# Kernel tuning notes

Hardware: AMD Instinct MI355X
Metric: run time of the kernel (lower is better)

## Reference

```python
import jax, jax.numpy as jnp
import numpy as np

SIGMA = 0.5
KS = 5  # gaussian kernel size, covers > 4*sigma


def _gauss_kernel():
    x = jnp.arange(KS, dtype=jnp.float32) - (KS // 2)
    g = jnp.exp(-(x ** 2) / (2.0 * SIGMA ** 2))
    k2 = jnp.outer(g, g)
    return k2 / k2.sum()


def setup_inputs() -> dict:
    key = jax.random.key(0)
    k1, k2, k3, k4 = jax.random.split(key, 4)
    B, K, H, W = 64, 17, 128, 128
    heatmap = jax.random.normal(k1, (B, K, H, W), dtype=jnp.float32)
    tx = jax.random.randint(k2, (B, K), 0, W)
    ty = jax.random.randint(k3, (B, K), 0, H)
    vis = jax.random.randint(k4, (B, K), 0, 2)
    targets = jnp.stack([tx, ty, vis], axis=-1).astype(jnp.float32)  # [B,K,3] = (x, y, visible)
    return {"heatmap": heatmap, "targets": targets}


def reference(heatmap, targets):
    B, K, H, W = heatmap.shape
    # log-softmax over flattened spatial dims
    logp = jax.nn.log_softmax(heatmap.reshape(B, K, H * W), axis=2).reshape(B, K, H, W)

    t = jnp.round(targets).astype(jnp.int32)
    visible = (t[..., 2] > 0).astype(logp.dtype)  # [B,K]
    tx, ty = t[..., 0], t[..., 1]

    # one-hot 2D heatmap at (ty, tx): [B,K,H,W]
    oh = ((jnp.arange(H)[:, None] == ty[..., None, None]) &
          (jnp.arange(W)[None, :] == tx[..., None, None])).astype(jnp.float32)

    # depthwise gaussian smoothing ('same' zero padding)
    kern = _gauss_kernel().reshape(1, 1, KS, KS)
    tgt = jax.lax.conv_general_dilated(
        oh.reshape(B * K, 1, H, W), kern,
        window_strides=(1, 1), padding='SAME',
        dimension_numbers=('NCHW', 'OIHW', 'NCHW')).reshape(B, K, H, W)

    # KLDiv pointwise: y*(log y - x); zero where y == 0 (torch convention)
    safe_t = jnp.where(tgt > 0, tgt, 1.0)
    elem = jnp.where(tgt > 0, tgt * (jnp.log(safe_t) - logp), 0.0)
    per_bk = elem.sum(axis=(-2, -1))  # [B,K]

    n_vis = jnp.maximum(visible.sum(), 1.0)
    loss = jnp.sum(per_bk * visible) / n_vis  # batchmean over visible keypoints
    return loss
```

## Files before the change

kernel.cpp:

```cpp
#include <hip/hip_runtime.h>
#include <math.h>

constexpr int Hc     = 128;
constexpr int Wc     = 128;
constexpr int HWc    = Hc * Wc;
constexpr int NBK    = 64 * 17;
constexpr int NCHUNK = 4;
constexpr int CHUNK  = HWc / NCHUNK;
constexpr int NBLK   = NBK * NCHUNK;

constexpr float E2_1 = 0.13533528323661270f;
constexpr float E2_4 = 3.3546262790251185e-4f;
constexpr float S1F  = 1.0f + 2.0f * E2_1 + 2.0f * E2_4;
constexpr float INVN = 1.0f / (S1F * S1F);

__device__ __forceinline__ float gfac(int d) {
    const int a = d < 0 ? -d : d;
    return a == 0 ? 1.0f : (a == 1 ? E2_1 : E2_4);
}

__global__ __launch_bounds__(256) void kl_chunk(const float* __restrict__ hm,
                                                const float* __restrict__ tg,
                                                float* __restrict__ part) {
    const int bx    = blockIdx.x;
    const int bk    = bx >> 2;
    const int chunk = bx & 3;
    const int tid   = threadIdx.x;

    const float4* __restrict__ base4 =
        reinterpret_cast<const float4*>(hm + (size_t)bk * HWc + (size_t)chunk * CHUNK);

    float s0 = 0.f, s1 = 0.f, s2 = 0.f, s3 = 0.f;
#pragma unroll
    for (int c = 0; c < 4; ++c) {
        const float4 v = base4[c * 256 + tid];
        s0 += __expf(v.x); s1 += __expf(v.y);
        s2 += __expf(v.z); s3 += __expf(v.w);
    }
    float s = (s0 + s1) + (s2 + s3);

    float gh = 0.f;
    if (tid < 25) {
        const int dy = tid / 5 - 2;
        const int dx = tid % 5 - 2;
        const int tx = __float2int_rn(tg[bk * 3 + 0]) + dx;
        const int ty = __float2int_rn(tg[bk * 3 + 1]) + dy;
        const int r0 = chunk * (Hc / NCHUNK);
        if (tx >= 0 && tx < Wc && ty >= r0 && ty < r0 + Hc / NCHUNK)
            gh = gfac(dx) * gfac(dy) * INVN * hm[(size_t)bk * HWc + ty * Wc + tx];
    }

#pragma unroll
    for (int off = 32; off; off >>= 1) s += __shfl_xor(s, off);
#pragma unroll
    for (int off = 16; off; off >>= 1) gh += __shfl_xor(gh, off);

    __shared__ float ss[4];
    const int wave = tid >> 6;
    if ((tid & 63) == 0) ss[wave] = s;
    __syncthreads();
    if (tid == 0) {
        part[bx]        = ss[0] + ss[1] + ss[2] + ss[3];
        part[NBLK + bx] = gh;
    }
}

__global__ __launch_bounds__(1024) void kl_final(const float* __restrict__ part,
                                                 const float* __restrict__ tg,
                                                 float* __restrict__ out) {
    const int tid = threadIdx.x;
    const float LOGN = 2.0f * __logf(S1F);

    float acc = 0.f, nv = 0.f;
    for (int i = tid; i < NBK; i += 1024) {
        const float4 sv = *reinterpret_cast<const float4*>(part + 4 * i);
        const float4 gv = *reinterpret_cast<const float4*>(part + NBLK + 4 * i);
        const float S   = (sv.x + sv.y) + (sv.z + sv.w);
        const float gh  = (gv.x + gv.y) + (gv.z + gv.w);
        const float lse = __logf(S);

        const int tx  = __float2int_rn(tg[3 * i + 0]);
        const int ty  = __float2int_rn(tg[3 * i + 1]);
        const int vis = __float2int_rn(tg[3 * i + 2]) > 0;

        float cg = 0.f, cglg = 0.f;
#pragma unroll
        for (int w = 0; w < 25; ++w) {
            const int dy = w / 5 - 2;
            const int dx = w % 5 - 2;
            const int x = tx + dx, y = ty + dy;
            if (x >= 0 && x < Wc && y >= 0 && y < Hc) {
                const float g = gfac(dx) * gfac(dy) * INVN;
                cg   += g;
                cglg += g * (-2.f * (float)(dx * dx + dy * dy) - LOGN);
            }
        }
        const float per = cglg - gh + lse * cg;
        acc += vis ? per : 0.f;
        nv  += vis ? 1.f : 0.f;
    }

#pragma unroll
    for (int off = 32; off; off >>= 1) {
        acc += __shfl_xor(acc, off);
        nv  += __shfl_xor(nv,  off);
    }
    __shared__ float sa[16], sn[16];
    const int wave = tid >> 6;
    if ((tid & 63) == 0) { sa[wave] = acc; sn[wave] = nv; }
    __syncthreads();
    if (tid == 0) {
        float a = 0.f, n = 0.f;
#pragma unroll
        for (int w = 0; w < 16; ++w) { a += sa[w]; n += sn[w]; }
        out[0] = a / fmaxf(n, 1.f);
    }
}

extern "C" void kernel_launch(void* const* d_in, const int* in_sizes, int n_in,
                              void* d_out, int out_size, void* d_ws, size_t ws_size,
                              hipStream_t stream) {
    const float* heatmap = (const float*)d_in[0];
    const float* targets = (const float*)d_in[1];
    float* part = (float*)d_ws;
    float* out  = (float*)d_out;

    kl_chunk<<<NBLK, 256, 0, stream>>>(heatmap, targets, part);
    kl_final<<<1, 1024, 0, stream>>>(part, targets, out);
}
```

Measured before the change: 19.46 us.

## Fuse chunk and final kernels into one cooperative launch with grid sync

Merges the two kernels into a single cooperative kernel. Each 1024-thread block now handles four whole (b,k) maps, computes the per-keypoint loss in-block, and writes one partial per block. After a grid-wide sync, block 0 reduces the partials and the visible count. This removes the second kernel launch and the small serial tail, at the cost of grid-sync overhead and a smaller grid (272 blocks) with more work per thread.

```diff
diff --git a/kernel.cpp b/kernel.cpp
--- a/kernel.cpp
+++ b/kernel.cpp
@@ -1,13 +1,15 @@
 #include <hip/hip_runtime.h>
+#include <hip/hip_cooperative_groups.h>
 #include <math.h>
 
-constexpr int Hc     = 128;
-constexpr int Wc     = 128;
-constexpr int HWc    = Hc * Wc;
-constexpr int NBK    = 64 * 17;
-constexpr int NCHUNK = 4;
-constexpr int CHUNK  = HWc / NCHUNK;
-constexpr int NBLK   = NBK * NCHUNK;
+namespace cg = cooperative_groups;
+
+constexpr int Hc   = 128;
+constexpr int Wc   = 128;
+constexpr int HWc  = Hc * Wc;
+constexpr int NBK  = 64 * 17;
+constexpr int RPB  = 4;
+constexpr int NBLK = NBK / RPB;
 
 constexpr float E2_1 = 0.13533528323661270f;
 constexpr float E2_4 = 3.3546262790251185e-4f;
@@ -19,34 +21,36 @@
     return a == 0 ? 1.0f : (a == 1 ? E2_1 : E2_4);
 }
 
-__global__ __launch_bounds__(256) void kl_chunk(const float* __restrict__ hm,
-                                                const float* __restrict__ tg,
-                                                float* __restrict__ part) {
-    const int bx    = blockIdx.x;
-    const int bk    = bx >> 2;
-    const int chunk = bx & 3;
-    const int tid   = threadIdx.x;
+__global__ __launch_bounds__(1024, 8) void kl_all(const float* __restrict__ hm,
+                                                  const float* __restrict__ tg,
+                                                  float* __restrict__ part,
+                                                  float* __restrict__ out) {
+    const int blk     = blockIdx.x;
+    const int tid     = threadIdx.x;
+    const int row     = tid >> 8;
+    const int lane256 = tid & 255;
+    const int bk      = blk * RPB + row;
+    const int wave    = tid >> 6;
 
     const float4* __restrict__ base4 =
-        reinterpret_cast<const float4*>(hm + (size_t)bk * HWc + (size_t)chunk * CHUNK);
+        reinterpret_cast<const float4*>(hm + (size_t)bk * HWc);
 
     float s0 = 0.f, s1 = 0.f, s2 = 0.f, s3 = 0.f;
-#pragma unroll
-    for (int c = 0; c < 4; ++c) {
-        const float4 v = base4[c * 256 + tid];
+#pragma unroll 4
+    for (int c = 0; c < 16; ++c) {
+        const float4 v = base4[c * 256 + lane256];
         s0 += __expf(v.x); s1 += __expf(v.y);
         s2 += __expf(v.z); s3 += __expf(v.w);
     }
     float s = (s0 + s1) + (s2 + s3);
 
     float gh = 0.f;
-    if (tid < 25) {
-        const int dy = tid / 5 - 2;
-        const int dx = tid % 5 - 2;
+    if (lane256 < 25) {
+        const int dy = lane256 / 5 - 2;
+        const int dx = lane256 % 5 - 2;
         const int tx = __float2int_rn(tg[bk * 3 + 0]) + dx;
         const int ty = __float2int_rn(tg[bk * 3 + 1]) + dy;
-        const int r0 = chunk * (Hc / NCHUNK);
-        if (tx >= 0 && tx < Wc && ty >= r0 && ty < r0 + Hc / NCHUNK)
+        if (tx >= 0 && tx < Wc && ty >= 0 && ty < Hc)
             gh = gfac(dx) * gfac(dy) * INVN * hm[(size_t)bk * HWc + ty * Wc + tx];
     }
 
@@ -55,35 +59,21 @@
 #pragma unroll
     for (int off = 16; off; off >>= 1) gh += __shfl_xor(gh, off);
 
-    __shared__ float ss[4];
-    const int wave = tid >> 6;
+    __shared__ float ss[16];
+    __shared__ float rowres[RPB];
     if ((tid & 63) == 0) ss[wave] = s;
     __syncthreads();
-    if (tid == 0) {
-        part[bx]        = ss[0] + ss[1] + ss[2] + ss[3];
-        part[NBLK + bx] = gh;
-    }
-}
 
-__global__ __launch_bounds__(1024) void kl_final(const float* __restrict__ part,
-                                                 const float* __restrict__ tg,
-                                                 float* __restrict__ out) {
-    const int tid = threadIdx.x;
-    const float LOGN = 2.0f * __logf(S1F);
-
-    float acc = 0.f, nv = 0.f;
-    for (int i = tid; i < NBK; i += 1024) {
-        const float4 sv = *reinterpret_cast<const float4*>(part + 4 * i);
-        const float4 gv = *reinterpret_cast<const float4*>(part + NBLK + 4 * i);
-        const float S   = (sv.x + sv.y) + (sv.z + sv.w);
-        const float gh  = (gv.x + gv.y) + (gv.z + gv.w);
+    if (lane256 == 0) {
+        const float S   = ss[4 * row] + ss[4 * row + 1] + ss[4 * row + 2] + ss[4 * row + 3];
         const float lse = __logf(S);
 
-        const int tx  = __float2int_rn(tg[3 * i + 0]);
-        const int ty  = __float2int_rn(tg[3 * i + 1]);
-        const int vis = __float2int_rn(tg[3 * i + 2]) > 0;
+        const int tx  = __float2int_rn(tg[bk * 3 + 0]);
+        const int ty  = __float2int_rn(tg[bk * 3 + 1]);
+        const int vis = __float2int_rn(tg[bk * 3 + 2]) > 0;
 
-        float cg = 0.f, cglg = 0.f;
+        const float LOGN = 2.0f * __logf(S1F);
+        float cgs = 0.f, cglg = 0.f;
 #pragma unroll
         for (int w = 0; w < 25; ++w) {
             const int dy = w / 5 - 2;
@@ -91,29 +81,37 @@
             const int x = tx + dx, y = ty + dy;
             if (x >= 0 && x < Wc && y >= 0 && y < Hc) {
                 const float g = gfac(dx) * gfac(dy) * INVN;
-                cg   += g;
+                cgs  += g;
                 cglg += g * (-2.f * (float)(dx * dx + dy * dy) - LOGN);
             }
         }
-        const float per = cglg - gh + lse * cg;
-        acc += vis ? per : 0.f;
-        nv  += vis ? 1.f : 0.f;
+        rowres[row] = vis ? (cglg - gh + lse * cgs) : 0.f;
     }
+    __syncthreads();
+    if (tid == 0)
+        part[blk] = (rowres[0] + rowres[1]) + (rowres[2] + rowres[3]);
+
+    cg::this_grid().sync();
+    if (blk != 0) return;
+
+    float a  = (tid < NBLK) ? part[tid] : 0.f;
+    float nv = (tid < NBK && __float2int_rn(tg[3 * tid + 2]) > 0) ? 1.f : 0.f;
+    if (tid < NBK - 1024)
+        nv += (__float2int_rn(tg[3 * (tid + 1024) + 2]) > 0) ? 1.f : 0.f;
 
 #pragma unroll
     for (int off = 32; off; off >>= 1) {
-        acc += __shfl_xor(acc, off);
-        nv  += __shfl_xor(nv,  off);
+        a  += __shfl_xor(a,  off);
+        nv += __shfl_xor(nv, off);
     }
     __shared__ float sa[16], sn[16];
-    const int wave = tid >> 6;
-    if ((tid & 63) == 0) { sa[wave] = acc; sn[wave] = nv; }
+    if ((tid & 63) == 0) { sa[wave] = a; sn[wave] = nv; }
     __syncthreads();
     if (tid == 0) {
-        float a = 0.f, n = 0.f;
+        a = 0.f; nv = 0.f;
 #pragma unroll
-        for (int w = 0; w < 16; ++w) { a += sa[w]; n += sn[w]; }
-        out[0] = a / fmaxf(n, 1.f);
+        for (int w = 0; w < 16; ++w) { a += sa[w]; nv += sn[w]; }
+        out[0] = a / fmaxf(nv, 1.f);
     }
 }
 
@@ -125,6 +123,7 @@
     float* part = (float*)d_ws;
     float* out  = (float*)d_out;
 
-    kl_chunk<<<NBLK, 256, 0, stream>>>(heatmap, targets, part);
-    kl_final<<<1, 1024, 0, stream>>>(part, targets, out);
+    void* args[] = {(void*)&heatmap, (void*)&targets, (void*)&part, (void*)&out};
+    hipLaunchCooperativeKernel((const void*)kl_all, dim3(NBLK), dim3(1024),
+                               args, 0, stream);
 }
```

Result: slower. 57.02 us (+193.0%).

## Fuse chunk and final kernels into one kernel with atomic accumulation

Applied to the files above, without the earlier changes.

Each block now handles a whole (b,k) heatmap instead of a quarter. It computes the log-sum-exp, the target gather and the per-keypoint loss in the block, then atomically adds the result scaled by 1/n_visible into the output. The second reduction kernel is gone, replaced by a memset plus per-block atomics, and every block recounts visible keypoints with one wave. The grid has 4x fewer blocks, each with 4x more work, which may reduce latency hiding, and float atomics make the summation order nondeterministic.

```diff
diff --git a/kernel.cpp b/kernel.cpp
--- a/kernel.cpp
+++ b/kernel.cpp
@@ -1,13 +1,10 @@
 #include <hip/hip_runtime.h>
 #include <math.h>
 
-constexpr int Hc     = 128;
-constexpr int Wc     = 128;
-constexpr int HWc    = Hc * Wc;
-constexpr int NBK    = 64 * 17;
-constexpr int NCHUNK = 4;
-constexpr int CHUNK  = HWc / NCHUNK;
-constexpr int NBLK   = NBK * NCHUNK;
+constexpr int Hc  = 128;
+constexpr int Wc  = 128;
+constexpr int HWc = Hc * Wc;
+constexpr int NBK = 64 * 17;
 
 constexpr float E2_1 = 0.13533528323661270f;
 constexpr float E2_4 = 3.3546262790251185e-4f;
@@ -19,20 +16,20 @@
     return a == 0 ? 1.0f : (a == 1 ? E2_1 : E2_4);
 }
 
-__global__ __launch_bounds__(256) void kl_chunk(const float* __restrict__ hm,
-                                                const float* __restrict__ tg,
-                                                float* __restrict__ part) {
-    const int bx    = blockIdx.x;
-    const int bk    = bx >> 2;
-    const int chunk = bx & 3;
-    const int tid   = threadIdx.x;
+__global__ __launch_bounds__(256) void kl_one(const float* __restrict__ hm,
+                                              const float* __restrict__ tg,
+                                              float* __restrict__ out) {
+    const int bk   = blockIdx.x;
+    const int tid  = threadIdx.x;
+    const int lane = tid & 63;
+    const int wave = tid >> 6;
 
     const float4* __restrict__ base4 =
-        reinterpret_cast<const float4*>(hm + (size_t)bk * HWc + (size_t)chunk * CHUNK);
+        reinterpret_cast<const float4*>(hm + (size_t)bk * HWc);
 
     float s0 = 0.f, s1 = 0.f, s2 = 0.f, s3 = 0.f;
 #pragma unroll
-    for (int c = 0; c < 4; ++c) {
+    for (int c = 0; c < 16; ++c) {
         const float4 v = base4[c * 256 + tid];
         s0 += __expf(v.x); s1 += __expf(v.y);
         s2 += __expf(v.z); s3 += __expf(v.w);
@@ -45,75 +42,57 @@
         const int dx = tid % 5 - 2;
         const int tx = __float2int_rn(tg[bk * 3 + 0]) + dx;
         const int ty = __float2int_rn(tg[bk * 3 + 1]) + dy;
-        const int r0 = chunk * (Hc / NCHUNK);
-        if (tx >= 0 && tx < Wc && ty >= r0 && ty < r0 + Hc / NCHUNK)
+        if (tx >= 0 && tx < Wc && ty >= 0 && ty < Hc)
             gh = gfac(dx) * gfac(dy) * INVN * hm[(size_t)bk * HWc + ty * Wc + tx];
     }
 
+    float nv = 0.f;
+    if (wave == 1) {
 #pragma unroll
-    for (int off = 32; off; off >>= 1) s += __shfl_xor(s, off);
-#pragma unroll
-    for (int off = 16; off; off >>= 1) gh += __shfl_xor(gh, off);
-
-    __shared__ float ss[4];
-    const int wave = tid >> 6;
-    if ((tid & 63) == 0) ss[wave] = s;
-    __syncthreads();
-    if (tid == 0) {
-        part[bx]        = ss[0] + ss[1] + ss[2] + ss[3];
-        part[NBLK + bx] = gh;
-    }
-}
-
-__global__ __launch_bounds__(1024) void kl_final(const float* __restrict__ part,
-                                                 const float* __restrict__ tg,
-                                                 float* __restrict__ out) {
-    const int tid = threadIdx.x;
-    const float LOGN = 2.0f * __logf(S1F);
-
-    float acc = 0.f, nv = 0.f;
-    for (int i = tid; i < NBK; i += 1024) {
-        const float4 sv = *reinterpret_cast<const float4*>(part + 4 * i);
-        const float4 gv = *reinterpret_cast<const float4*>(part + NBLK + 4 * i);
-        const float S   = (sv.x + sv.y) + (sv.z + sv.w);
-        const float gh  = (gv.x + gv.y) + (gv.z + gv.w);
-        const float lse = __logf(S);
-
-        const int tx  = __float2int_rn(tg[3 * i + 0]);
-        const int ty  = __float2int_rn(tg[3 * i + 1]);
-        const int vis = __float2int_rn(tg[3 * i + 2]) > 0;
-
-        float cg = 0.f, cglg = 0.f;
-#pragma unroll
-        for (int w = 0; w < 25; ++w) {
-            const int dy = w / 5 - 2;
-            const int dx = w % 5 - 2;
-            const int x = tx + dx, y = ty + dy;
-            if (x >= 0 && x < Wc && y >= 0 && y < Hc) {
-                const float g = gfac(dx) * gfac(dy) * INVN;
-                cg   += g;
-                cglg += g * (-2.f * (float)(dx * dx + dy * dy) - LOGN);
-            }
-        }
-        const float per = cglg - gh + lse * cg;
-        acc += vis ? per : 0.f;
-        nv  += vis ? 1.f : 0.f;
+        for (int i = 0; i < NBK / 64; ++i)
+            nv += (__float2int_rn(tg[3 * (lane + 64 * i) + 2]) > 0) ? 1.f : 0.f;
     }
 
 #pragma unroll
     for (int off = 32; off; off >>= 1) {
-        acc += __shfl_xor(acc, off);
-        nv  += __shfl_xor(nv,  off);
+        s  += __shfl_xor(s,  off);
+        gh += __shfl_xor(gh, off);
+        nv += __shfl_xor(nv, off);
     }
-    __shared__ float sa[16], sn[16];
-    const int wave = tid >> 6;
-    if ((tid & 63) == 0) { sa[wave] = acc; sn[wave] = nv; }
+
+    __shared__ float ss[4];
+    __shared__ float sG, sNV;
+    if (lane == 0) {
+        ss[wave] = s;
+        if (wave == 0) sG  = gh;
+        if (wave == 1) sNV = nv;
+    }
     __syncthreads();
+
     if (tid == 0) {
-        float a = 0.f, n = 0.f;
+        const int vis = __float2int_rn(tg[bk * 3 + 2]) > 0;
+        if (vis) {
+            const float S   = (ss[0] + ss[1]) + (ss[2] + ss[3]);
+            const float lse = __logf(S);
+            const int tx = __float2int_rn(tg[bk * 3 + 0]);
+            const int ty = __float2int_rn(tg[bk * 3 + 1]);
+
+            const float LOGN = 2.0f * __logf(S1F);
+            float cg = 0.f, cglg = 0.f;
 #pragma unroll
-        for (int w = 0; w < 16; ++w) { a += sa[w]; n += sn[w]; }
-        out[0] = a / fmaxf(n, 1.f);
+            for (int w = 0; w < 25; ++w) {
+                const int dy = w / 5 - 2;
+                const int dx = w % 5 - 2;
+                const int x = tx + dx, y = ty + dy;
+                if (x >= 0 && x < Wc && y >= 0 && y < Hc) {
+                    const float g = gfac(dx) * gfac(dy) * INVN;
+                    cg   += g;
+                    cglg += g * (-2.f * (float)(dx * dx + dy * dy) - LOGN);
+                }
+            }
+            const float per = cglg - sG + lse * cg;
+            atomicAdd(out, per / fmaxf(sNV, 1.f));
+        }
     }
 }
 
@@ -122,9 +101,8 @@
                               hipStream_t stream) {
     const float* heatmap = (const float*)d_in[0];
     const float* targets = (const float*)d_in[1];
-    float* part = (float*)d_ws;
-    float* out  = (float*)d_out;
+    float* out = (float*)d_out;
 
-    kl_chunk<<<NBLK, 256, 0, stream>>>(heatmap, targets, part);
-    kl_final<<<1, 1024, 0, stream>>>(part, targets, out);
+    hipMemsetAsync(out, 0, sizeof(float), stream);
+    kl_one<<<NBK, 256, 0, stream>>>(heatmap, targets, out);
 }
```

New measurement: 26.72 us. +37.3%, slower.
